# Performance work log

Hardware: AMD Instinct MI355X
Metric: run time of the kernel (lower is better)

## Reference

```python
import jax, jax.numpy as jnp
import numpy as np

FACTOR = 5

def setup_inputs() -> dict:
    key = jax.random.key(0)
    k1, k2, k3 = jax.random.split(key, 3)
    B, L, H, D = 4, 2048, 8, 64
    logL = int(np.ceil(np.log(L)))          # 8
    U_part = min(2 * FACTOR * logL, L)      # 80 sampled keys per query
    queries = jax.random.normal(k1, (B, L, H, D), dtype=jnp.float32)
    keys = jax.random.normal(k2, (B, L, H, D), dtype=jnp.float32)
    index_sample = jax.random.randint(k3, (L, U_part), 0, L)
    return {"queries": queries, "keys": keys, "index_sample": index_sample}

def reference(queries, keys, index_sample):
    B, L, H, D = queries.shape
    q = jnp.transpose(queries, (0, 2, 1, 3))   # [B,H,L,D]
    k = jnp.transpose(keys, (0, 2, 1, 3))      # [B,H,L,D]
    logL = int(np.ceil(np.log(L)))
    u = min(FACTOR * logL, L)                  # n_top queries

    # sample keys per query position: [B,H,L,S,D]
    K_sample = k[:, :, index_sample, :]
    # Q_i . K_sample_ij : [B,H,L,S]
    QK_sample = jnp.einsum('bhld,bhlsd->bhls', q, K_sample)
    # sparsity measure M = max - mean (mean over full L as in source)
    M = QK_sample.max(axis=-1) - QK_sample.sum(axis=-1) / L   # [B,H,L]
    _, M_top = jax.lax.top_k(M, u)                            # [B,H,u]

    # gather selected queries and compute full scores against all keys
    Q_reduce = jnp.take_along_axis(q, M_top[..., None], axis=2)  # [B,H,u,D]
    scale = 1.0 / jnp.sqrt(jnp.float32(D))
    scores = jnp.einsum('bhud,bhld->bhul', Q_reduce, k) * scale  # [B,H,u,L]
    attn = jax.nn.softmax(scores, axis=-1)

    # scatter softmaxed rows into full [B,H,L,L] attention matrix (rest zeros)
    out = jnp.zeros((B, H, L, L), dtype=attn.dtype)
    b_idx = jnp.arange(B)[:, None, None]
    h_idx = jnp.arange(H)[None, :, None]
    out = out.at[b_idx, h_idx, M_top, :].set(attn)
    return out
```

## Files before the change

kernel.cpp:

```cpp
#include <hip/hip_runtime.h>
#include <math.h>

#define NB 4
#define NL 2048
#define NH 8
#define ND 64
#define NUPART 80
#define NUTOP 40
#define ZROWS1 1800

typedef float vfloat4 __attribute__((ext_vector_type(4)));

__global__ __launch_bounds__(256) void k_compute_M_zero(
    const float* __restrict__ q, const float* __restrict__ k,
    const int* __restrict__ idx, float* __restrict__ M,
    float* __restrict__ out)
{
    const int t = threadIdx.x;

    {
        const int bhz = blockIdx.x >> 9;
        const int j   = blockIdx.x & 511;
        vfloat4* o = (vfloat4*)out + (size_t)bhz * (NL * (ND * 8)) + j * 1800 + t;
        const vfloat4 z = (vfloat4)(0.0f);
#pragma unroll
        for (int i = 0; i < 7; ++i) o[i * 256] = z;
        if (t < 8) o[7 * 256] = z;
    }

    const int w    = blockIdx.x * 4 + (t >> 6);
    const int lane = t & 63;
    const int l    = w & (NL - 1);
    const int bh   = w >> 11;
    const int h    = bh & (NH - 1);
    const int b    = bh >> 3;
    const int sl   = lane >> 2;
    const int dg   = lane & 3;
    const int d0   = dg * 16;

    const float4* qv = (const float4*)(q + (((size_t)(b * NL + l) * NH + h) * ND + d0));
    const float4 q0 = qv[0], q1 = qv[1], q2 = qv[2], q3 = qv[3];

    float mx = -INFINITY, sm = 0.0f;
#pragma unroll
    for (int r = 0; r < 5; ++r) {
        const int s  = r * 16 + sl;
        const int ki = idx[l * NUPART + s];
        const float4* kv = (const float4*)(k + (((size_t)(b * NL + ki) * NH + h) * ND + d0));
        const float4 k0 = kv[0], k1 = kv[1], k2 = kv[2], k3 = kv[3];
        float p = q0.x * k0.x + q0.y * k0.y + q0.z * k0.z + q0.w * k0.w
                + q1.x * k1.x + q1.y * k1.y + q1.z * k1.z + q1.w * k1.w
                + q2.x * k2.x + q2.y * k2.y + q2.z * k2.z + q2.w * k2.w
                + q3.x * k3.x + q3.y * k3.y + q3.z * k3.z + q3.w * k3.w;
        p += __shfl_xor(p, 1);
        p += __shfl_xor(p, 2);
        mx = fmaxf(mx, p);
        sm += p;
    }
#pragma unroll
    for (int m = 4; m < 64; m <<= 1) {
        mx = fmaxf(mx, __shfl_xor(mx, m));
        sm += __shfl_xor(sm, m);
    }
    if (lane == 0) M[w] = mx - sm * (1.0f / (float)NL);
}

__global__ __launch_bounds__(256) void k_topk(
    const float* __restrict__ M, int* __restrict__ rowmap,
    int* __restrict__ Mtop)
{
    __shared__ float sM[NL];
    __shared__ float rv[4];
    __shared__ int   ri[4];
    const int bh = blockIdx.x;
    const int t  = threadIdx.x;

    for (int j = t; j < NL; j += 256) {
        sM[j] = M[bh * NL + j];
        rowmap[bh * NL + j] = 0;
    }
    __syncthreads();

    for (int it = 0; it < NUTOP; ++it) {
        float v = -INFINITY;
        int   i = NL;
        for (int j = t; j < NL; j += 256) {
            const float m = sM[j];
            if (m > v || (m == v && j < i)) { v = m; i = j; }
        }
#pragma unroll
        for (int off = 1; off < 64; off <<= 1) {
            const float ov = __shfl_xor(v, off);
            const int   oi = __shfl_xor(i, off);
            if (ov > v || (ov == v && oi < i)) { v = ov; i = oi; }
        }
        const int wid = t >> 6;
        if ((t & 63) == 0) { rv[wid] = v; ri[wid] = i; }
        __syncthreads();
        if (t == 0) {
            for (int w2 = 1; w2 < 4; ++w2) {
                if (rv[w2] > v || (rv[w2] == v && ri[w2] < i)) { v = rv[w2]; i = ri[w2]; }
            }
            Mtop[bh * NUTOP + it] = i;
            rowmap[bh * NL + i] = 1;
            sM[i] = -INFINITY;
        }
        __syncthreads();
    }
}

__global__ __launch_bounds__(256) void k_attn_zero(
    const float* __restrict__ q, const float* __restrict__ k,
    const int* __restrict__ rowmap, const int* __restrict__ Mtop,
    float* __restrict__ out)
{
    const int bh  = blockIdx.x / NUTOP;
    const int ui  = blockIdx.x % NUTOP;
    const int b   = bh >> 3;
    const int h   = bh & 7;
    const int t   = threadIdx.x;
    const int row = Mtop[bh * NUTOP + ui];

    {
        const vfloat4 z = (vfloat4)(0.0f);
        int r0, nr;
        if (ui < 8) { r0 = ZROWS1 + ui * 7; nr = 7; }
        else        { r0 = ZROWS1 + 56 + (ui - 8) * 6; nr = 6; }
        for (int rr = 0; rr < nr; ++rr) {
            const int rz = r0 + rr;
            if (rowmap[bh * NL + rz]) continue;
            vfloat4* o = (vfloat4*)out + ((size_t)bh * NL + rz) * (NL / 4) + t;
            o[0]   = z;
            o[256] = z;
        }
    }

    __shared__ float redm[4];
    __shared__ float reds[4];
    const int lane = t & 63;
    const int wid  = t >> 6;

    const float4* qv = (const float4*)(q + (((size_t)(b * NL + row)) * NH + h) * ND);
    float4 qr[16];
#pragma unroll
    for (int i = 0; i < 16; ++i) qr[i] = qv[i];

    float sc[8];
    float mx = -INFINITY;
#pragma unroll
    for (int j = 0; j < 8; ++j) {
        const int l = t + 256 * j;
        const float4* kv = (const float4*)(k + (((size_t)(b * NL + l)) * NH + h) * ND);
        float s = 0.0f;
#pragma unroll
        for (int i = 0; i < 16; ++i) {
            const float4 kk = kv[i];
            s += qr[i].x * kk.x + qr[i].y * kk.y + qr[i].z * kk.z + qr[i].w * kk.w;
        }
        sc[j] = s * 0.125f;
        mx = fmaxf(mx, sc[j]);
    }

#pragma unroll
    for (int off = 1; off < 64; off <<= 1) mx = fmaxf(mx, __shfl_xor(mx, off));
    if (lane == 0) redm[wid] = mx;
    __syncthreads();
    mx = fmaxf(fmaxf(redm[0], redm[1]), fmaxf(redm[2], redm[3]));

    float lsum = 0.0f;
#pragma unroll
    for (int j = 0; j < 8; ++j) {
        sc[j] = __expf(sc[j] - mx);
        lsum += sc[j];
    }
#pragma unroll
    for (int off = 1; off < 64; off <<= 1) lsum += __shfl_xor(lsum, off);
    if (lane == 0) reds[wid] = lsum;
    __syncthreads();
    const float inv = 1.0f / (reds[0] + reds[1] + reds[2] + reds[3]);

    float* orow = out + ((size_t)bh * NL + row) * NL;
#pragma unroll
    for (int j = 0; j < 8; ++j) {
        orow[t + 256 * j] = sc[j] * inv;
    }
}

extern "C" void kernel_launch(void* const* d_in, const int* in_sizes, int n_in,
                              void* d_out, int out_size, void* d_ws, size_t ws_size,
                              hipStream_t stream) {
    const float* q   = (const float*)d_in[0];
    const float* k   = (const float*)d_in[1];
    const int*   idx = (const int*)d_in[2];
    float* out = (float*)d_out;

    float* Mws    = (float*)d_ws;
    int*   rowmap = (int*)((char*)d_ws + (size_t)NB * NH * NL * 4);
    int*   Mtop   = (int*)((char*)d_ws + (size_t)NB * NH * NL * 8);

    k_compute_M_zero<<<NB * NH * NL / 4, 256, 0, stream>>>(q, k, idx, Mws, out);
    k_topk<<<NB * NH, 256, 0, stream>>>(Mws, rowmap, Mtop);
    k_attn_zero<<<NB * NH * NUTOP, 256, 0, stream>>>(q, k, rowmap, Mtop, out);
}
```

Baseline: 379.4 us.

## Move most output zero-fill from first kernel into dedicated blocks of attention kernel

The first kernel now zeroes only the first 320 rows per (b,h) instead of 1800. The remaining 1728 rows are zeroed by extra dedicated blocks appended to the attention kernel's grid, which skip rows that top-k selected. This shifts the bulk of the 512 MB output write into the final kernel, which can also skip the selected rows. The first kernel becomes lighter, but the zero-fill now runs after top-k and can no longer overlap with the M computation.

```diff
diff --git a/kernel.cpp b/kernel.cpp
--- a/kernel.cpp
+++ b/kernel.cpp
@@ -7,7 +7,9 @@
 #define ND 64
 #define NUPART 80
 #define NUTOP 40
-#define ZROWS1 1800
+#define ZROWS_K1 320
+#define NZB_PER_BH 432
+#define NATTN (NB * NH * NUTOP)
 
 typedef float vfloat4 __attribute__((ext_vector_type(4)));
 
@@ -21,11 +23,10 @@
     {
         const int bhz = blockIdx.x >> 9;
         const int j   = blockIdx.x & 511;
-        vfloat4* o = (vfloat4*)out + (size_t)bhz * (NL * (ND * 8)) + j * 1800 + t;
+        vfloat4* o = (vfloat4*)out + (size_t)bhz * (NL * NL / 4) + j * 320 + t;
         const vfloat4 z = (vfloat4)(0.0f);
-#pragma unroll
-        for (int i = 0; i < 7; ++i) o[i * 256] = z;
-        if (t < 8) o[7 * 256] = z;
+        o[0] = z;
+        if (t < 64) o[256] = z;
     }
 
     const int w    = blockIdx.x * 4 + (t >> 6);
@@ -114,26 +115,30 @@
     const int* __restrict__ rowmap, const int* __restrict__ Mtop,
     float* __restrict__ out)
 {
+    const int t = threadIdx.x;
+
+    if (blockIdx.x >= NATTN) {
+        const int zb = blockIdx.x - NATTN;
+        const int bh = zb / NZB_PER_BH;
+        const int ri = zb - bh * NZB_PER_BH;
+        const int r0 = ZROWS_K1 + ri * 4;
+        const vfloat4 z = (vfloat4)(0.0f);
+#pragma unroll
+        for (int rr = 0; rr < 4; ++rr) {
+            const int r = r0 + rr;
+            if (rowmap[bh * NL + r]) continue;
+            vfloat4* o = (vfloat4*)out + ((size_t)bh * NL + r) * (NL / 4) + t;
+            o[0]   = z;
+            o[256] = z;
+        }
+        return;
+    }
+
     const int bh  = blockIdx.x / NUTOP;
     const int ui  = blockIdx.x % NUTOP;
     const int b   = bh >> 3;
     const int h   = bh & 7;
-    const int t   = threadIdx.x;
     const int row = Mtop[bh * NUTOP + ui];
-
-    {
-        const vfloat4 z = (vfloat4)(0.0f);
-        int r0, nr;
-        if (ui < 8) { r0 = ZROWS1 + ui * 7; nr = 7; }
-        else        { r0 = ZROWS1 + 56 + (ui - 8) * 6; nr = 6; }
-        for (int rr = 0; rr < nr; ++rr) {
-            const int rz = r0 + rr;
-            if (rowmap[bh * NL + rz]) continue;
-            vfloat4* o = (vfloat4*)out + ((size_t)bh * NL + rz) * (NL / 4) + t;
-            o[0]   = z;
-            o[256] = z;
-        }
-    }
 
     __shared__ float redm[4];
     __shared__ float reds[4];
@@ -200,5 +205,5 @@
 
     k_compute_M_zero<<<NB * NH * NL / 4, 256, 0, stream>>>(q, k, idx, Mws, out);
     k_topk<<<NB * NH, 256, 0, stream>>>(Mws, rowmap, Mtop);
-    k_attn_zero<<<NB * NH * NUTOP, 256, 0, stream>>>(q, k, rowmap, Mtop, out);
-}
+    k_attn_zero<<<NATTN + NB * NH * NZB_PER_BH, 256, 0, stream>>>(q, k, rowmap, Mtop, out);
+}
```

New measurement: 403.4 us. 6.3% more time.
